# Optimization experiments

Measured on AMD Instinct MI355X. Metric: run time of the kernel, lower is better.

The kernel has to match this reference:

```python
import jax, jax.numpy as jnp
import numpy as np

H = 2048      # hidden
QL = 768      # q lora rank
KVL = 512     # kv lora rank
DR = 64       # rope dim
DN = 128      # nope head dim
NH = 16       # attention heads
NIH = 8       # indexer heads
IDX = 128     # indexer key dim
BS = 16       # batch
BLK = 128     # cache block size
BPS = 32      # blocks per sequence
NB = BS * BPS # total cache blocks
MAXKV = BPS * BLK  # 4096 kv slots per seq
TOPK = 1024   # sparse attention budget


def rmsnorm(v, g, eps=1e-6):
    return v * jax.lax.rsqrt(jnp.mean(v * v, -1, keepdims=True) + eps) * g


def layernorm(v, g, b, eps=1e-6):
    c = v - jnp.mean(v, -1, keepdims=True)
    return c * jax.lax.rsqrt(jnp.mean(c * c, -1, keepdims=True) + eps) * g + b


def rope(v, sin, cos):
    h = v.shape[-1] // 2
    rot = jnp.concatenate([-v[..., h:], v[..., :h]], -1)
    return v * cos + rot * sin


def setup_inputs() -> dict:
    key = jax.random.key(0)
    ks = jax.random.split(key, 16)
    s = 0.02  # weight init scale
    ang = jax.random.uniform(ks[5], (BS, 1, DR)) * 6.2831853
    return dict(
        x=jax.random.normal(ks[0], (BS, 1, H)),
        w_dq=jax.random.normal(ks[1], (H, QL)) * s,
        w_uq_qr=jax.random.normal(ks[2], (QL, NH * (DN + DR))) * s,
        w_uk=jax.random.normal(ks[3], (NH, DN, KVL)) * s,
        w_dkv_kr=jax.random.normal(ks[4], (H, KVL + DR)) * s,
        gamma_cq=jnp.ones((QL,)),
        gamma_ckv=jnp.ones((KVL,)),
        sin=jnp.sin(ang),
        cos=jnp.cos(ang),
        cache_index=jnp.arange(BS, dtype=jnp.int32) * MAXKV,
        kv_cache=jax.random.normal(ks[6], (NB, BLK, KVL)),
        kr_cache=jax.random.normal(ks[7], (NB, BLK, DR)),
        block_table=jnp.arange(BS * BPS, dtype=jnp.int32).reshape(BS, BPS),
        act_seqs=jnp.full((BS,), MAXKV, dtype=jnp.int32),
        w_idx_qb=jax.random.normal(ks[8], (QL, NIH * IDX)) * s,
        w_idx_k=jax.random.normal(ks[9], (H, IDX)) * s,
        w_idx_proj=jax.random.normal(ks[10], (QL, NIH)) * s,
        in_gamma_k=jnp.ones((IDX,)),
        in_beta_k=jnp.zeros((IDX,)),
        index_k_cache=jax.random.normal(ks[11], (NB, BLK, IDX)),
    )


def reference(x, w_dq, w_uq_qr, w_uk, w_dkv_kr, gamma_cq, gamma_ckv, sin, cos,
              cache_index, kv_cache, kr_cache, block_table, act_seqs,
              w_idx_qb, w_idx_k, w_idx_proj, in_gamma_k, in_beta_k, index_k_cache):
    bs = x.shape[0]
    xq = x[:, 0]                      # [bs, H] (decode, q_len=1)
    s0, c0 = sin[:, 0], cos[:, 0]     # [bs, DR]

    # --- low-rank Q path ---
    cq = rmsnorm(xq @ w_dq, gamma_cq)                           # [bs, QL]
    q = (cq @ w_uq_qr).reshape(bs, NH, DN + DR)
    q_nope, q_pe = q[..., :DN], q[..., DN:]
    q_pe = rope(q_pe, s0[:, None, :], c0[:, None, :])           # [bs, NH, DR]

    # --- latent KV path + cache write ---
    ckv_kr = xq @ w_dkv_kr
    ckv = rmsnorm(ckv_kr[:, :KVL], gamma_ckv)                   # [bs, KVL]
    kr = rope(ckv_kr[:, KVL:], s0, c0)                          # [bs, DR]
    kv_flat = kv_cache.reshape(NB * BLK, KVL).at[cache_index].set(ckv)
    kr_flat = kr_cache.reshape(NB * BLK, DR).at[cache_index].set(kr)

    # --- lightning indexer ---
    ki = layernorm(xq @ w_idx_k, in_gamma_k, in_beta_k)         # [bs, IDX]
    ik_flat = index_k_cache.reshape(NB * BLK, IDX).at[cache_index].set(ki)
    qi = (cq @ w_idx_qb).reshape(bs, NIH, IDX)
    head_w = cq @ w_idx_proj                                    # [bs, NIH]

    # paged gather: flat slot ids per sequence position
    pos = (block_table * BLK)[:, :, None] + jnp.arange(BLK, dtype=block_table.dtype)
    pos = pos.reshape(bs, MAXKV)                                # [bs, MAXKV]
    ki_all = ik_flat[pos]                                       # [bs, MAXKV, IDX]

    isc = jax.nn.relu(jnp.einsum('bhd,bnd->bhn', qi, ki_all))
    isc = jnp.einsum('bh,bhn->bn', head_w, isc) / jnp.sqrt(jnp.float32(IDX))
    mask = jnp.arange(MAXKV)[None, :] < act_seqs[:, None]
    isc = jnp.where(mask, isc, -1e9)
    top_s, top_i = jax.lax.top_k(isc, TOPK)                     # [bs, TOPK]

    sel = jnp.take_along_axis(pos, top_i, axis=1)               # [bs, TOPK]
    ckv_sel = kv_flat[sel]                                      # [bs, TOPK, KVL]
    kr_sel = kr_flat[sel]                                       # [bs, TOPK, DR]

    # --- absorbed MLA attention over selected tokens ---
    q_lat = jnp.einsum('bhd,hdc->bhc', q_nope, w_uk)            # [bs, NH, KVL]
    scale = 1.0 / np.sqrt(DN + DR)
    att = (jnp.einsum('bhc,bnc->bhn', q_lat, ckv_sel)
           + jnp.einsum('bhr,bnr->bhn', q_pe, kr_sel)) * scale
    att = jnp.where((top_s > -1e8)[:, None, :], att, -1e9)
    p = jax.nn.softmax(att, axis=-1)                            # [bs, NH, TOPK]
    o_lat = jnp.einsum('bhn,bnc->bhc', p, ckv_sel)              # [bs, NH, KVL]
    o = jnp.einsum('bhc,hdc->bhd', o_lat, w_uk)                 # [bs, NH, DN]
    return o.reshape(bs, 1, NH * DN)
```

## Files before the change

kernel.cpp:

```cpp
#include <hip/hip_runtime.h>

typedef unsigned int u32;

#define BS    16
#define HDIM  2048
#define QL    768
#define KVL   512
#define DR    64
#define DN    128
#define NH    16
#define NIH   8
#define IDXD  128
#define BLK   128
#define BPS   32
#define MAXKV 4096
#define TOPK  1024
#define NCH   32

__global__ void k_dproj(const float* __restrict__ x, const float* __restrict__ w_dq,
                        const float* __restrict__ w_dkv, const float* __restrict__ w_ik,
                        float* __restrict__ dpart){
  int tile = blockIdx.x, ks = blockIdx.y, t = threadIdx.x;
  __shared__ float xs[16*128];
  __shared__ float sred[8*32*17];
  int k0 = ks*128;
  for (int idx=t; idx<16*128; idx+=256){
    int bb=idx>>7, kk=idx&127;
    xs[idx] = x[bb*HDIM + k0 + kk];
  }
  const float* wp; int ld, c0, gbase;
  if (tile < 24){ wp=w_dq;  ld=768; c0=tile*32;      gbase=0; }
  else if (tile < 42){ wp=w_dkv; ld=576; c0=(tile-24)*32; gbase=768; }
  else { wp=w_ik;  ld=128; c0=(tile-42)*32; gbase=1344; }
  int cl = t&31, kg = t>>5;
  int col = c0 + cl;
  __syncthreads();
  float acc[16];
  #pragma unroll
  for (int bb=0;bb<16;bb++) acc[bb]=0.f;
  const float* wb = wp + (size_t)(k0 + kg*16)*ld + col;
  #pragma unroll 4
  for (int kk=0; kk<16; kk++){
    float wv = wb[(size_t)kk*ld];
    int kx = kg*16+kk;
    #pragma unroll
    for (int bb=0; bb<16; bb++) acc[bb] += xs[bb*128+kx]*wv;
  }
  #pragma unroll
  for (int bb=0;bb<16;bb++) sred[(kg*32+cl)*17+bb] = acc[bb];
  __syncthreads();
  for (int r=0; r<2; r++){
    int o = r*256 + t;
    int bb = o>>5, cl2 = o&31;
    float s=0.f;
    #pragma unroll
    for (int kg2=0; kg2<8; kg2++) s += sred[(kg2*32+cl2)*17+bb];
    dpart[((size_t)ks*16 + bb)*1472 + gbase + c0 + cl2] = s;
  }
}

__global__ void k_dfin(const float* __restrict__ dpart, const float* __restrict__ g_cq,
                       const float* __restrict__ g_ckv, const float* __restrict__ sinp,
                       const float* __restrict__ cosp, const float* __restrict__ g_ik,
                       const float* __restrict__ b_ik, const int* __restrict__ cidx,
                       float* __restrict__ cq, float* __restrict__ kvc,
                       float* __restrict__ krc, float* __restrict__ ikc){
  int b = blockIdx.x, sec = blockIdx.y, t = threadIdx.x;
  __shared__ float val[768];
  __shared__ float red[256];
  if (sec==0){
    for (int c=t; c<768; c+=256){
      float s = 0.f;
      for (int ks2=0; ks2<16; ks2++) s += dpart[((size_t)ks2*16+b)*1472 + c];
      val[c] = s;
    }
    __syncthreads();
    float c0v = val[t], c1v = val[t+256], c2v = val[t+512];
    red[t] = c0v*c0v + c1v*c1v + c2v*c2v;
    __syncthreads();
    for (int s=128;s>0;s>>=1){ if(t<s) red[t]+=red[t+s]; __syncthreads(); }
    float scq = 1.0f/sqrtf(red[0]/(float)QL + 1e-6f);
    cq[b*QL+t]     = c0v*scq*g_cq[t];
    cq[b*QL+t+256] = c1v*scq*g_cq[t+256];
    cq[b*QL+t+512] = c2v*scq*g_cq[t+512];
  } else if (sec==1){
    for (int c=t; c<576; c+=256){
      float s = 0.f;
      for (int ks2=0; ks2<16; ks2++) s += dpart[((size_t)ks2*16+b)*1472 + 768 + c];
      val[c] = s;
    }
    __syncthreads();
    float v0 = val[t], v1 = val[t+256];
    red[t] = v0*v0 + v1*v1;
    __syncthreads();
    for (int s=128;s>0;s>>=1){ if(t<s) red[t]+=red[t+s]; __syncthreads(); }
    float sckv = 1.0f/sqrtf(red[0]/(float)KVL + 1e-6f);
    int ci = cidx[b];
    kvc[(size_t)ci*KVL + t]     = v0*sckv*g_ckv[t];
    kvc[(size_t)ci*KVL + t+256] = v1*sckv*g_ckv[t+256];
    if (t<DR){
      float v = val[512+t];
      float rot = (t<32)? -val[512+t+32] : val[512+t-32];
      krc[(size_t)ci*DR + t] = v*cosp[b*DR+t] + rot*sinp[b*DR+t];
    }
  } else {
    for (int c=t; c<128; c+=256){
      float s = 0.f;
      for (int ks2=0; ks2<16; ks2++) s += dpart[((size_t)ks2*16+b)*1472 + 1344 + c];
      val[c] = s;
    }
    __syncthreads();
    red[t] = (t<128)? val[t] : 0.f;
    __syncthreads();
    for (int s=128;s>0;s>>=1){ if(t<s) red[t]+=red[t+s]; __syncthreads(); }
    float mean = red[0]/(float)IDXD;
    __syncthreads();
    float cc = (t<128)? (val[t]-mean) : 0.f;
    red[t] = cc*cc;
    __syncthreads();
    for (int s=128;s>0;s>>=1){ if(t<s) red[t]+=red[t+s]; __syncthreads(); }
    float var = red[0]/(float)IDXD;
    int ci = cidx[b];
    if (t<IDXD){
      ikc[(size_t)ci*IDXD + t] = cc/sqrtf(var+1e-6f)*g_ik[t] + b_ik[t];
    }
  }
}

__global__ void k_qall(const float* __restrict__ cq, const float* __restrict__ w_uq,
                       const float* __restrict__ w_qb, const float* __restrict__ w_pj,
                       float* __restrict__ qpart){
  int tile = blockIdx.x, ks = blockIdx.y, t = threadIdx.x;
  __shared__ float xs[16*192];
  __shared__ float sred[8*32*17];
  int k0 = ks*192;
  for (int idx=t; idx<16*192; idx+=256){
    int bb = idx/192, kk = idx - bb*192;
    xs[idx] = cq[bb*QL + k0 + kk];
  }
  const float* wp; int ld, c0, gbase, kind;
  if (tile < 96){ wp=w_uq; ld=3072; c0=tile*32; gbase=0; kind=0; }
  else if (tile < 128){ wp=w_qb; ld=1024; c0=(tile-96)*32; gbase=3072; kind=0; }
  else { wp=w_pj; ld=8; c0=0; gbase=4096; kind=1; }
  int cl = t&31, kg = t>>5;
  int col = c0 + cl;
  bool act = !(kind==1 && cl>=8);
  __syncthreads();
  float acc[16];
  #pragma unroll
  for (int bb=0;bb<16;bb++) acc[bb]=0.f;
  const float* wb = wp + (size_t)(k0 + kg*24)*ld + col;
  if (act){
    #pragma unroll 4
    for (int kk=0; kk<24; kk++){
      float wv = wb[(size_t)kk*ld];
      int kx = kg*24+kk;
      #pragma unroll
      for (int bb=0; bb<16; bb++) acc[bb] += xs[bb*192+kx]*wv;
    }
  }
  #pragma unroll
  for (int bb=0;bb<16;bb++) sred[(kg*32+cl)*17+bb] = acc[bb];
  __syncthreads();
  for (int r=0; r<2; r++){
    int o = r*256 + t;
    int bb = o>>5, cl2 = o&31;
    float s=0.f;
    #pragma unroll
    for (int kg2=0; kg2<8; kg2++) s += sred[(kg2*32+cl2)*17+bb];
    qpart[((size_t)ks*16 + bb)*4128 + gbase + c0 + cl2] = s;
  }
}

__global__ void k_qfin(const float* __restrict__ qpart, const float* __restrict__ sinp,
                       const float* __restrict__ cosp, float* __restrict__ qn,
                       float* __restrict__ qp, float* __restrict__ qi,
                       float* __restrict__ hw){
  int b=blockIdx.x, part=blockIdx.y, t=threadIdx.x;
  if (part<16){
    __shared__ float val[192];
    int h=part;
    if (t<192){
      int c = h*192 + t;
      float s=0.f;
      for (int ks=0; ks<4; ks++) s += qpart[((size_t)ks*16+b)*4128 + c];
      val[t]=s;
    }
    __syncthreads();
    if (t<192){
      int j=t;
      if (j<128) qn[(b*NH+h)*DN+j] = val[j];
      else {
        int d=j-128;
        float v=val[j];
        float rot = (d<32)? -val[160+d] : val[96+d];
        qp[(b*NH+h)*DR+d] = v*cosp[b*DR+d] + rot*sinp[b*DR+d];
      }
    }
  } else {
    for (int idx=t; idx<1032; idx+=256){
      int c = 3072+idx;
      float s=0.f;
      for (int ks=0; ks<4; ks++) s += qpart[((size_t)ks*16+b)*4128 + c];
      if (idx<1024) qi[b*1024 + idx] = s;
      else hw[b*NIH + idx-1024] = s;
    }
  }
}

__global__ void k_qlat(const float* __restrict__ qn, const float* __restrict__ wuk,
                       float* __restrict__ ql){
  int h=blockIdx.x, ct=blockIdx.y, t=threadIdx.x;
  __shared__ float qs[16*128];
  __shared__ float sred[4*64*17];
  for (int idx=t; idx<2048; idx+=256)
    qs[idx] = qn[((idx>>7)*NH+h)*DN + (idx&127)];
  int cl=t&63, kg=t>>6;
  int col=ct*64+cl;
  __syncthreads();
  float acc[16];
  #pragma unroll
  for (int bb=0;bb<16;bb++) acc[bb]=0.f;
  const float* wb = wuk + ((size_t)h*DN + kg*32)*KVL + col;
  #pragma unroll 4
  for (int kk=0;kk<32;kk++){
    float wv = wb[(size_t)kk*KVL];
    int kx = kg*32+kk;
    #pragma unroll
    for (int bb=0;bb<16;bb++) acc[bb]+=qs[bb*128+kx]*wv;
  }
  #pragma unroll
  for (int bb=0;bb<16;bb++) sred[(kg*64+cl)*17+bb]=acc[bb];
  __syncthreads();
  for (int r=0;r<4;r++){
    int o=r*256+t;
    int bb=o>>6, cl2=o&63;
    float s=0.f;
    #pragma unroll
    for (int kg2=0;kg2<4;kg2++) s+=sred[(kg2*64+cl2)*17+bb];
    ql[((size_t)bb*NH+h)*KVL + ct*64+cl2] = s;
  }
}

__global__ void k_isc(const float* __restrict__ qi, const float* __restrict__ hw,
                      const float* __restrict__ ikc, const int* __restrict__ btab,
                      const int* __restrict__ aseq, float* __restrict__ isc){
  int b=blockIdx.x, jb=blockIdx.y, t=threadIdx.x;
  __shared__ float K[64*129];
  __shared__ float qs[NIH*130];
  __shared__ float hs[NIH];
  __shared__ float red[64*4];
  int blk = btab[b*BPS+jb];
  for (int idx=t; idx<NIH*IDXD; idx+=256){ int h2=idx>>7, d=idx&127; qs[h2*130+d]=qi[b*1024+idx]; }
  if (t<NIH) hs[t]=hw[b*NIH+t];
  const float4* k4 = (const float4*)(ikc + (size_t)blk*BLK*IDXD);
  int as = aseq[b];
  int r = t>>2, hp = t&3;
  for (int half=0; half<2; half++){
    __syncthreads();
    for (int it=0; it<8; it++){
      int idx = it*256 + t;
      int rr = idx>>5, c4 = idx&31;
      float4 v = k4[(half*64+rr)*32 + c4];
      float* dst = &K[rr*129 + c4*4];
      dst[0]=v.x; dst[1]=v.y; dst[2]=v.z; dst[3]=v.w;
    }
    __syncthreads();
    float s0=0.f, s1=0.f;
    const float* Kr = &K[r*129];
    const float* q0 = &qs[hp*130];
    const float* q1 = &qs[(hp+4)*130];
    for (int d=0; d<IDXD; d++){
      float kv = Kr[d];
      s0 += q0[d]*kv; s1 += q1[d]*kv;
    }
    red[r*4+hp] = hs[hp]*fmaxf(s0,0.f) + hs[hp+4]*fmaxf(s1,0.f);
    __syncthreads();
    if (t<64){
      float sc = (red[t*4]+red[t*4+1]+red[t*4+2]+red[t*4+3]) * 0.08838834764831845f;
      int n = jb*BLK + half*64 + t;
      if (n >= as) sc = -1e9f;
      isc[b*MAXKV + n] = sc;
    }
  }
}

__global__ void k_topk(const float* __restrict__ isc, const int* __restrict__ btab,
                       int* __restrict__ selp, float* __restrict__ sels){
  int b=blockIdx.x, t=threadIdx.x;
  int lane = t&63, wv = t>>6;
  __shared__ u32 su[MAXKV];
  __shared__ u32 hist[256];
  __shared__ u32 cum[256];
  __shared__ u32 wtot[4];
  __shared__ u32 sh_b;
  for (int k2=0;k2<16;k2++){
    int i=k2*256+t;
    u32 bits=__float_as_uint(isc[b*MAXKV+i]);
    su[i] = (bits & 0x80000000u) ? ~bits : (bits | 0x80000000u);
  }
  u32 prefix=0u, need=1024u;
  for (int shift=24; shift>=0; shift-=8){
    hist[t]=0u;
    __syncthreads();
    u32 hm = (shift==24)? 0u : (0xFFFFFFFFu << (shift+8));
    for (int j=0;j<16;j++){
      u32 u = su[t*16+j];
      if ((u & hm) == prefix) atomicAdd(&hist[(u>>shift)&255u], 1u);
    }
    __syncthreads();
    u32 v = hist[wv*64+lane];
    for (int off=1; off<64; off<<=1){
      u32 tmp = __shfl_down(v, off);
      if (lane + off < 64) v += tmp;
    }
    if (lane==0) wtot[wv]=v;
    __syncthreads();
    u32 add=0u;
    for (int w2=wv+1; w2<4; w2++) add += wtot[w2];
    v += add;
    cum[wv*64+lane] = v;
    __syncthreads();
    int bin = wv*64+lane;
    u32 nxt = (bin<255)? cum[bin+1] : 0u;
    if (v>=need && nxt<need) sh_b = (u32)bin;
    __syncthreads();
    u32 B = sh_b;
    u32 aboveB = (B<255u)? cum[B+1] : 0u;
    need -= aboveB;
    prefix |= (B<<shift);
    __syncthreads();
  }
  u32 T = prefix;
  u32 cG=0u,cE=0u;
  for (int j=0;j<16;j++){ u32 u=su[t*16+j]; cG += (u>T)?1u:0u; cE += (u==T)?1u:0u; }
  u32 packed = (cG<<16) | cE;
  u32 v = packed;
  for (int off=1; off<64; off<<=1){
    u32 tmp = __shfl_up(v, off);
    if (lane >= off) v += tmp;
  }
  if (lane==63) wtot[wv]=v;
  __syncthreads();
  u32 add=0u;
  for (int w2=0; w2<wv; w2++) add += wtot[w2];
  u32 excl = v + add - packed;
  u32 total = wtot[0]+wtot[1]+wtot[2]+wtot[3];
  u32 mGT = total>>16;
  u32 keepEq = 1024u - mGT;
  u32 gG = excl>>16, gE = excl&0xFFFFu;
  for (int j=0;j<16;j++){
    int i=t*16+j; u32 u=su[i];
    int slot=-1;
    if (u>T) slot=(int)(gG++);
    else if (u==T){ u32 r2=gE++; if (r2<keepEq) slot=(int)(mGT+r2); }
    if (slot>=0){
      int pos = btab[b*BPS + (i>>7)]*BLK + (i&127);
      selp[b*TOPK+slot]=pos;
      sels[b*TOPK+slot]=isc[b*MAXKV+i];
    }
  }
}

__global__ __launch_bounds__(256, 2)
void k_fgat(const float* __restrict__ qlat, const float* __restrict__ qpe,
            const float* __restrict__ kvc, const float* __restrict__ krc,
            const int* __restrict__ selp, const float* __restrict__ sels,
            float* __restrict__ opart, float* __restrict__ mch,
            float* __restrict__ lch){
  int ch=blockIdx.x, b=blockIdx.y, t=threadIdx.x;
  __shared__ float K[32*580];
  int lane31 = t&31;
  int sp_l   = selp[b*TOPK + ch*32 + lane31];
  float sv_l = sels[b*TOPK + ch*32 + lane31];
  const float4* kv4 = (const float4*)kvc;
  const float4* kr4 = (const float4*)krc;
  float4 rA[18];
  #pragma unroll
  for (int j=0;j<18;j++){
    int idx=j*256+t, r=idx/144, c=idx-r*144;
    int row = __shfl(sp_l, r, 64);
    rA[j] = (c<128)? kv4[(size_t)row*128 + c] : kr4[(size_t)row*16 + (c-128)];
  }
  int h = t>>4, kc = t&15;
  const float4* ql4 = (const float4*)(qlat + ((size_t)b*NH+h)*KVL);
  const float4* qp4 = (const float4*)(qpe  + ((size_t)b*NH+h)*DR);
  float4 qreg[9];
  #pragma unroll
  for (int j=0;j<9;j++){
    int g = kc*9 + j;
    qreg[j] = (g<128)? ql4[g] : qp4[g-128];
  }
  #pragma unroll
  for (int j=0;j<18;j++){
    int idx=j*256+t, r=idx/144, c=idx-r*144;
    ((float4*)&K[r*580])[c] = rA[j];
  }
  __syncthreads();
  const float scale = 0.07216878364870323f;
  float pa=0.f, pb=0.f;
  for (int r=0;r<32;r++){
    const float4* Kc = (const float4*)&K[r*580 + kc*36];
    float s=0.f;
    #pragma unroll
    for (int j=0;j<9;j++){
      float4 kv=Kc[j], q=qreg[j];
      s += kv.x*q.x + kv.y*q.y + kv.z*q.z + kv.w*q.w;
    }
    #pragma unroll
    for (int mm=1;mm<16;mm<<=1) s += __shfl_xor(s, mm, 16);
    float svr = __shfl(sv_l, r, 64);
    float val = (svr > -1e8f)? s*scale : -1e9f;
    if (r<16) pa = (kc==r)?      val : pa;
    else      pb = (kc==(r-16))? val : pb;
  }
  float m2 = fmaxf(pa, pb);
  #pragma unroll
  for (int mm=1;mm<16;mm<<=1) m2 = fmaxf(m2, __shfl_xor(m2, mm, 16));
  pa = expf(pa - m2); pb = expf(pb - m2);
  float l2 = pa + pb;
  #pragma unroll
  for (int mm=1;mm<16;mm<<=1) l2 += __shfl_xor(l2, mm, 16);
  int l6 = t&63;
  float4 a0[4], a1[4];
  #pragma unroll
  for (int hq=0;hq<4;hq++){
    a0[hq].x=a0[hq].y=a0[hq].z=a0[hq].w=0.f;
    a1[hq].x=a1[hq].y=a1[hq].z=a1[hq].w=0.f;
  }
  for (int r=0;r<32;r++){
    const float4* Vr = (const float4*)&K[r*580];
    float4 v0 = Vr[l6], v1 = Vr[64+l6];
    float ps = (r<16)? pa : pb;
    int srcl = (r&15);
    float p0 = __shfl(ps, srcl,      64);
    float p1 = __shfl(ps, 16+srcl,   64);
    float p2 = __shfl(ps, 32+srcl,   64);
    float p3 = __shfl(ps, 48+srcl,   64);
    a0[0].x+=p0*v0.x; a0[0].y+=p0*v0.y; a0[0].z+=p0*v0.z; a0[0].w+=p0*v0.w;
    a1[0].x+=p0*v1.x; a1[0].y+=p0*v1.y; a1[0].z+=p0*v1.z; a1[0].w+=p0*v1.w;
    a0[1].x+=p1*v0.x; a0[1].y+=p1*v0.y; a0[1].z+=p1*v0.z; a0[1].w+=p1*v0.w;
    a1[1].x+=p1*v1.x; a1[1].y+=p1*v1.y; a1[1].z+=p1*v1.z; a1[1].w+=p1*v1.w;
    a0[2].x+=p2*v0.x; a0[2].y+=p2*v0.y; a0[2].z+=p2*v0.z; a0[2].w+=p2*v0.w;
    a1[2].x+=p2*v1.x; a1[2].y+=p2*v1.y; a1[2].z+=p2*v1.z; a1[2].w+=p2*v1.w;
    a0[3].x+=p3*v0.x; a0[3].y+=p3*v0.y; a0[3].z+=p3*v0.z; a0[3].w+=p3*v0.w;
    a1[3].x+=p3*v1.x; a1[3].y+=p3*v1.y; a1[3].z+=p3*v1.z; a1[3].w+=p3*v1.w;
  }
  int wv = t>>6;
  #pragma unroll
  for (int hq=0;hq<4;hq++){
    int hh = wv*4 + hq;
    float4* dst = (float4*)(opart + (((size_t)(b*NCH+ch))*NH + hh)*KVL);
    dst[l6]    = a0[hq];
    dst[64+l6] = a1[hq];
  }
  if (kc==0){
    mch[(b*NCH+ch)*16 + h] = m2;
    lch[(b*NCH+ch)*16 + h] = l2;
  }
}

__global__ void k_comb(const float* __restrict__ opart, const float* __restrict__ mch,
                       const float* __restrict__ lch, const float* __restrict__ wuk,
                       float* __restrict__ out){
  int b=blockIdx.x, h=blockIdx.y, t=threadIdx.x;
  __shared__ float sOl[KVL];
  __shared__ float sCoef[NCH];
  __shared__ float sInvL;
  if (t<NCH){
    float mv = mch[(b*NCH+t)*16+h];
    float lv = lch[(b*NCH+t)*16+h];
    float M = mv;
    for (int off=1; off<NCH; off<<=1) M = fmaxf(M, __shfl_xor(M, off, NCH));
    float coef = expf(mv - M);
    float Lp = lv*coef;
    for (int off=1; off<NCH; off<<=1) Lp += __shfl_xor(Lp, off, NCH);
    sCoef[t] = coef;
    if (t==0) sInvL = 1.0f/Lp;
  }
  __syncthreads();
  for (int c=t; c<KVL; c+=128){
    float s=0.f;
    for (int ch=0; ch<NCH; ch++)
      s += opart[(((size_t)(b*NCH+ch))*NH + h)*KVL + c] * sCoef[ch];
    sOl[c] = s*sInvL;
  }
  __syncthreads();
  const float4* w4 = (const float4*)(wuk + ((size_t)(h*DN)+t)*KVL);
  const float4* o4 = (const float4*)sOl;
  float a=0.f;
  for (int v=0; v<128; v++){
    float4 w = w4[v]; float4 o = o4[v];
    a += w.x*o.x + w.y*o.y + w.z*o.z + w.w*o.w;
  }
  out[b*(NH*DN) + h*DN + t] = a;
}

extern "C" void kernel_launch(void* const* d_in, const int* in_sizes, int n_in,
                              void* d_out, int out_size, void* d_ws, size_t ws_size,
                              hipStream_t stream){
  const float* x        =(const float*)d_in[0];
  const float* w_dq     =(const float*)d_in[1];
  const float* w_uq_qr  =(const float*)d_in[2];
  const float* w_uk     =(const float*)d_in[3];
  const float* w_dkv_kr =(const float*)d_in[4];
  const float* g_cq     =(const float*)d_in[5];
  const float* g_ckv    =(const float*)d_in[6];
  const float* sinp     =(const float*)d_in[7];
  const float* cosp     =(const float*)d_in[8];
  const int*   cidx     =(const int*)d_in[9];
  float*       kvc      =(float*)d_in[10];
  float*       krc      =(float*)d_in[11];
  const int*   btab     =(const int*)d_in[12];
  const int*   aseq     =(const int*)d_in[13];
  const float* w_idx_qb =(const float*)d_in[14];
  const float* w_idx_k  =(const float*)d_in[15];
  const float* w_idx_pj =(const float*)d_in[16];
  const float* g_ik     =(const float*)d_in[17];
  const float* b_ik     =(const float*)d_in[18];
  float*       ikc      =(float*)d_in[19];

  float* ws    = (float*)d_ws;
  float* cq    = ws;
  float* qnope = ws + 12288;
  float* qpe   = ws + 45056;
  float* qlat  = ws + 61440;
  float* qi    = ws + 192512;
  float* hw    = ws + 208896;
  float* isc   = ws + 209024;
  int*   selp  = (int*)(ws + 274560);
  float* sels  = ws + 290944;
  float* dpart = ws + 307328;
  float* qpart = ws + 684160;
  float* mch   = ws + 948352;
  float* lch   = ws + 956544;
  float* opart = ws + 964736;

  k_dproj<<<dim3(46,16),  dim3(256),0,stream>>>(x,w_dq,w_dkv_kr,w_idx_k,dpart);
  k_dfin <<<dim3(BS,3),   dim3(256),0,stream>>>(dpart,g_cq,g_ckv,sinp,cosp,g_ik,b_ik,cidx,cq,kvc,krc,ikc);
  k_qall <<<dim3(129,4),  dim3(256),0,stream>>>(cq,w_uq_qr,w_idx_qb,w_idx_pj,qpart);
  k_qfin <<<dim3(BS,17),  dim3(256),0,stream>>>(qpart,sinp,cosp,qnope,qpe,qi,hw);
  k_qlat <<<dim3(16,8),   dim3(256),0,stream>>>(qnope,w_uk,qlat);
  k_isc  <<<dim3(BS,BPS), dim3(256),0,stream>>>(qi,hw,ikc,btab,aseq,isc);
  k_topk <<<dim3(BS),     dim3(256),0,stream>>>(isc,btab,selp,sels);
  k_fgat <<<dim3(NCH,BS), dim3(256),0,stream>>>(qlat,qpe,kvc,krc,selp,sels,opart,mch,lch);
  k_comb <<<dim3(BS,NH),  dim3(128),0,stream>>>(opart,mch,lch,w_uk,(float*)d_out);
}
```

Measured before the change: 344.7 us.

## Fuse q-latent projection into qfin, stop writing cache, tweak isc/topk

Folds the per-head w_uk projection into k_qfin, removing the k_qlat launch and the q_nope round trip. The new kv/kr/index-key rows are now written to workspace and substituted on read in k_isc and k_fgat, instead of being scattered into the input caches. k_isc also gains float4 shared-memory loads with padded rows, and k_topk uses 16 privatized histogram copies with strided element ownership to cut atomic contention. The fused qlat computation redoes the w_uk read once per batch row (16x more weight traffic) in exchange for one fewer launch.

```diff
diff --git a/kernel.cpp b/kernel.cpp
--- a/kernel.cpp
+++ b/kernel.cpp
@@ -62,9 +62,9 @@
 __global__ void k_dfin(const float* __restrict__ dpart, const float* __restrict__ g_cq,
                        const float* __restrict__ g_ckv, const float* __restrict__ sinp,
                        const float* __restrict__ cosp, const float* __restrict__ g_ik,
-                       const float* __restrict__ b_ik, const int* __restrict__ cidx,
-                       float* __restrict__ cq, float* __restrict__ kvc,
-                       float* __restrict__ krc, float* __restrict__ ikc){
+                       const float* __restrict__ b_ik,
+                       float* __restrict__ cq, float* __restrict__ newkv,
+                       float* __restrict__ newkr, float* __restrict__ newik){
   int b = blockIdx.x, sec = blockIdx.y, t = threadIdx.x;
   __shared__ float val[768];
   __shared__ float red[256];
@@ -95,13 +95,12 @@
     __syncthreads();
     for (int s=128;s>0;s>>=1){ if(t<s) red[t]+=red[t+s]; __syncthreads(); }
     float sckv = 1.0f/sqrtf(red[0]/(float)KVL + 1e-6f);
-    int ci = cidx[b];
-    kvc[(size_t)ci*KVL + t]     = v0*sckv*g_ckv[t];
-    kvc[(size_t)ci*KVL + t+256] = v1*sckv*g_ckv[t+256];
+    newkv[(size_t)b*KVL + t]     = v0*sckv*g_ckv[t];
+    newkv[(size_t)b*KVL + t+256] = v1*sckv*g_ckv[t+256];
     if (t<DR){
       float v = val[512+t];
       float rot = (t<32)? -val[512+t+32] : val[512+t-32];
-      krc[(size_t)ci*DR + t] = v*cosp[b*DR+t] + rot*sinp[b*DR+t];
+      newkr[(size_t)b*DR + t] = v*cosp[b*DR+t] + rot*sinp[b*DR+t];
     }
   } else {
     for (int c=t; c<128; c+=256){
@@ -120,9 +119,8 @@
     __syncthreads();
     for (int s=128;s>0;s>>=1){ if(t<s) red[t]+=red[t+s]; __syncthreads(); }
     float var = red[0]/(float)IDXD;
-    int ci = cidx[b];
     if (t<IDXD){
-      ikc[(size_t)ci*IDXD + t] = cc/sqrtf(var+1e-6f)*g_ik[t] + b_ik[t];
+      newik[(size_t)b*IDXD + t] = cc/sqrtf(var+1e-6f)*g_ik[t] + b_ik[t];
     }
   }
 }
@@ -173,9 +171,9 @@
 }
 
 __global__ void k_qfin(const float* __restrict__ qpart, const float* __restrict__ sinp,
-                       const float* __restrict__ cosp, float* __restrict__ qn,
-                       float* __restrict__ qp, float* __restrict__ qi,
-                       float* __restrict__ hw){
+                       const float* __restrict__ cosp, const float* __restrict__ wuk,
+                       float* __restrict__ qp, float* __restrict__ qlat,
+                       float* __restrict__ qi, float* __restrict__ hw){
   int b=blockIdx.x, part=blockIdx.y, t=threadIdx.x;
   if (part<16){
     __shared__ float val[192];
@@ -187,16 +185,22 @@
       val[t]=s;
     }
     __syncthreads();
-    if (t<192){
-      int j=t;
-      if (j<128) qn[(b*NH+h)*DN+j] = val[j];
-      else {
-        int d=j-128;
-        float v=val[j];
-        float rot = (d<32)? -val[160+d] : val[96+d];
-        qp[(b*NH+h)*DR+d] = v*cosp[b*DR+d] + rot*sinp[b*DR+d];
-      }
-    }
+    if (t>=128 && t<192){
+      int d=t-128;
+      float v=val[t];
+      float rot = (d<32)? -val[160+d] : val[96+d];
+      qp[(b*NH+h)*DR+d] = v*cosp[b*DR+d] + rot*sinp[b*DR+d];
+    }
+    float a0=0.f, a1=0.f;
+    const float* w = wuk + (size_t)h*DN*KVL;
+    #pragma unroll 4
+    for (int d=0; d<128; d++){
+      float qv = val[d];
+      a0 += qv * w[(size_t)d*KVL + t];
+      a1 += qv * w[(size_t)d*KVL + t + 256];
+    }
+    qlat[((size_t)b*NH+h)*KVL + t]       = a0;
+    qlat[((size_t)b*NH+h)*KVL + t + 256] = a1;
   } else {
     for (int idx=t; idx<1032; idx+=256){
       int c = 3072+idx;
@@ -208,52 +212,21 @@
   }
 }
 
-__global__ void k_qlat(const float* __restrict__ qn, const float* __restrict__ wuk,
-                       float* __restrict__ ql){
-  int h=blockIdx.x, ct=blockIdx.y, t=threadIdx.x;
-  __shared__ float qs[16*128];
-  __shared__ float sred[4*64*17];
-  for (int idx=t; idx<2048; idx+=256)
-    qs[idx] = qn[((idx>>7)*NH+h)*DN + (idx&127)];
-  int cl=t&63, kg=t>>6;
-  int col=ct*64+cl;
-  __syncthreads();
-  float acc[16];
-  #pragma unroll
-  for (int bb=0;bb<16;bb++) acc[bb]=0.f;
-  const float* wb = wuk + ((size_t)h*DN + kg*32)*KVL + col;
-  #pragma unroll 4
-  for (int kk=0;kk<32;kk++){
-    float wv = wb[(size_t)kk*KVL];
-    int kx = kg*32+kk;
-    #pragma unroll
-    for (int bb=0;bb<16;bb++) acc[bb]+=qs[bb*128+kx]*wv;
-  }
-  #pragma unroll
-  for (int bb=0;bb<16;bb++) sred[(kg*64+cl)*17+bb]=acc[bb];
-  __syncthreads();
-  for (int r=0;r<4;r++){
-    int o=r*256+t;
-    int bb=o>>6, cl2=o&63;
-    float s=0.f;
-    #pragma unroll
-    for (int kg2=0;kg2<4;kg2++) s+=sred[(kg2*64+cl2)*17+bb];
-    ql[((size_t)bb*NH+h)*KVL + ct*64+cl2] = s;
-  }
-}
-
 __global__ void k_isc(const float* __restrict__ qi, const float* __restrict__ hw,
                       const float* __restrict__ ikc, const int* __restrict__ btab,
-                      const int* __restrict__ aseq, float* __restrict__ isc){
+                      const int* __restrict__ aseq, const int* __restrict__ cidx,
+                      const float* __restrict__ newik, float* __restrict__ isc){
   int b=blockIdx.x, jb=blockIdx.y, t=threadIdx.x;
-  __shared__ float K[64*129];
-  __shared__ float qs[NIH*130];
+  __shared__ float K[64*132];
+  __shared__ float qs[NIH*132];
   __shared__ float hs[NIH];
   __shared__ float red[64*4];
   int blk = btab[b*BPS+jb];
-  for (int idx=t; idx<NIH*IDXD; idx+=256){ int h2=idx>>7, d=idx&127; qs[h2*130+d]=qi[b*1024+idx]; }
+  int ci  = cidx[b];
+  for (int idx=t; idx<NIH*IDXD; idx+=256){ int h2=idx>>7, d=idx&127; qs[h2*132+d]=qi[b*1024+idx]; }
   if (t<NIH) hs[t]=hw[b*NIH+t];
-  const float4* k4 = (const float4*)(ikc + (size_t)blk*BLK*IDXD);
+  const float4* k4   = (const float4*)(ikc + (size_t)blk*BLK*IDXD);
+  const float4* nik4 = (const float4*)(newik + (size_t)b*IDXD);
   int as = aseq[b];
   int r = t>>2, hp = t&3;
   for (int half=0; half<2; half++){
@@ -261,18 +234,21 @@
     for (int it=0; it<8; it++){
       int idx = it*256 + t;
       int rr = idx>>5, c4 = idx&31;
-      float4 v = k4[(half*64+rr)*32 + c4];
-      float* dst = &K[rr*129 + c4*4];
-      dst[0]=v.x; dst[1]=v.y; dst[2]=v.z; dst[3]=v.w;
+      int grow = blk*BLK + half*64 + rr;
+      float4 v = (grow==ci)? nik4[c4] : k4[(half*64+rr)*32 + c4];
+      ((float4*)&K[rr*132])[c4] = v;
     }
     __syncthreads();
     float s0=0.f, s1=0.f;
-    const float* Kr = &K[r*129];
-    const float* q0 = &qs[hp*130];
-    const float* q1 = &qs[(hp+4)*130];
-    for (int d=0; d<IDXD; d++){
-      float kv = Kr[d];
-      s0 += q0[d]*kv; s1 += q1[d]*kv;
+    const float4* Kr = (const float4*)&K[r*132];
+    const float4* q0 = (const float4*)&qs[hp*132];
+    const float4* q1 = (const float4*)&qs[(hp+4)*132];
+    for (int d=0; d<32; d++){
+      float4 kv=Kr[d], a=q0[d], c=q1[d];
+      s0 += a.x*kv.x; s1 += c.x*kv.x;
+      s0 += a.y*kv.y; s1 += c.y*kv.y;
+      s0 += a.z*kv.z; s1 += c.z*kv.z;
+      s0 += a.w*kv.w; s1 += c.w*kv.w;
     }
     red[r*4+hp] = hs[hp]*fmaxf(s0,0.f) + hs[hp+4]*fmaxf(s1,0.f);
     __syncthreads();
@@ -290,26 +266,30 @@
   int b=blockIdx.x, t=threadIdx.x;
   int lane = t&63, wv = t>>6;
   __shared__ u32 su[MAXKV];
-  __shared__ u32 hist[256];
+  __shared__ u32 hist[16*256];
   __shared__ u32 cum[256];
   __shared__ u32 wtot[4];
   __shared__ u32 sh_b;
-  for (int k2=0;k2<16;k2++){
-    int i=k2*256+t;
+  int hc = (t&15)*256;
+  for (int j=0;j<16;j++){
+    int i=j*256+t;
     u32 bits=__float_as_uint(isc[b*MAXKV+i]);
     su[i] = (bits & 0x80000000u) ? ~bits : (bits | 0x80000000u);
   }
   u32 prefix=0u, need=1024u;
   for (int shift=24; shift>=0; shift-=8){
-    hist[t]=0u;
+    for (int j=t;j<16*256;j+=256) hist[j]=0u;
     __syncthreads();
     u32 hm = (shift==24)? 0u : (0xFFFFFFFFu << (shift+8));
     for (int j=0;j<16;j++){
-      u32 u = su[t*16+j];
-      if ((u & hm) == prefix) atomicAdd(&hist[(u>>shift)&255u], 1u);
-    }
-    __syncthreads();
-    u32 v = hist[wv*64+lane];
+      u32 u = su[j*256+t];
+      if ((u & hm) == prefix) atomicAdd(&hist[hc + ((u>>shift)&255u)], 1u);
+    }
+    __syncthreads();
+    int bin = wv*64+lane;
+    u32 v = 0u;
+    #pragma unroll
+    for (int cpy=0;cpy<16;cpy++) v += hist[cpy*256+bin];
     for (int off=1; off<64; off<<=1){
       u32 tmp = __shfl_down(v, off);
       if (lane + off < 64) v += tmp;
@@ -319,9 +299,8 @@
     u32 add=0u;
     for (int w2=wv+1; w2<4; w2++) add += wtot[w2];
     v += add;
-    cum[wv*64+lane] = v;
-    __syncthreads();
-    int bin = wv*64+lane;
+    cum[bin] = v;
+    __syncthreads();
     u32 nxt = (bin<255)? cum[bin+1] : 0u;
     if (v>=need && nxt<need) sh_b = (u32)bin;
     __syncthreads();
@@ -333,7 +312,7 @@
   }
   u32 T = prefix;
   u32 cG=0u,cE=0u;
-  for (int j=0;j<16;j++){ u32 u=su[t*16+j]; cG += (u>T)?1u:0u; cE += (u==T)?1u:0u; }
+  for (int j=0;j<16;j++){ u32 u=su[j*256+t]; cG += (u>T)?1u:0u; cE += (u==T)?1u:0u; }
   u32 packed = (cG<<16) | cE;
   u32 v = packed;
   for (int off=1; off<64; off<<=1){
@@ -350,7 +329,7 @@
   u32 keepEq = 1024u - mGT;
   u32 gG = excl>>16, gE = excl&0xFFFFu;
   for (int j=0;j<16;j++){
-    int i=t*16+j; u32 u=su[i];
+    int i=j*256+t; u32 u=su[i];
     int slot=-1;
     if (u>T) slot=(int)(gG++);
     else if (u==T){ u32 r2=gE++; if (r2<keepEq) slot=(int)(mGT+r2); }
@@ -366,6 +345,8 @@
 void k_fgat(const float* __restrict__ qlat, const float* __restrict__ qpe,
             const float* __restrict__ kvc, const float* __restrict__ krc,
             const int* __restrict__ selp, const float* __restrict__ sels,
+            const int* __restrict__ cidx, const float* __restrict__ newkv,
+            const float* __restrict__ newkr,
             float* __restrict__ opart, float* __restrict__ mch,
             float* __restrict__ lch){
   int ch=blockIdx.x, b=blockIdx.y, t=threadIdx.x;
@@ -373,14 +354,20 @@
   int lane31 = t&31;
   int sp_l   = selp[b*TOPK + ch*32 + lane31];
   float sv_l = sels[b*TOPK + ch*32 + lane31];
-  const float4* kv4 = (const float4*)kvc;
-  const float4* kr4 = (const float4*)krc;
+  int ci = cidx[b];
+  const float4* kv4  = (const float4*)kvc;
+  const float4* kr4  = (const float4*)krc;
+  const float4* nkv4 = (const float4*)newkv;
+  const float4* nkr4 = (const float4*)newkr;
   float4 rA[18];
   #pragma unroll
   for (int j=0;j<18;j++){
     int idx=j*256+t, r=idx/144, c=idx-r*144;
     int row = __shfl(sp_l, r, 64);
-    rA[j] = (c<128)? kv4[(size_t)row*128 + c] : kr4[(size_t)row*16 + (c-128)];
+    const float4* src;
+    if (c<128) src = (row==ci)? (nkv4 + (size_t)b*128 + c) : (kv4 + (size_t)row*128 + c);
+    else       src = (row==ci)? (nkr4 + (size_t)b*16 + (c-128)) : (kr4 + (size_t)row*16 + (c-128));
+    rA[j] = *src;
   }
   int h = t>>4, kc = t&15;
   const float4* ql4 = (const float4*)(qlat + ((size_t)b*NH+h)*KVL);
@@ -509,8 +496,8 @@
   const float* sinp     =(const float*)d_in[7];
   const float* cosp     =(const float*)d_in[8];
   const int*   cidx     =(const int*)d_in[9];
-  float*       kvc      =(float*)d_in[10];
-  float*       krc      =(float*)d_in[11];
+  const float* kvc      =(const float*)d_in[10];
+  const float* krc      =(const float*)d_in[11];
   const int*   btab     =(const int*)d_in[12];
   const int*   aseq     =(const int*)d_in[13];
   const float* w_idx_qb =(const float*)d_in[14];
@@ -518,31 +505,32 @@
   const float* w_idx_pj =(const float*)d_in[16];
   const float* g_ik     =(const float*)d_in[17];
   const float* b_ik     =(const float*)d_in[18];
-  float*       ikc      =(float*)d_in[19];
+  const float* ikc      =(const float*)d_in[19];
 
   float* ws    = (float*)d_ws;
   float* cq    = ws;
-  float* qnope = ws + 12288;
-  float* qpe   = ws + 45056;
-  float* qlat  = ws + 61440;
-  float* qi    = ws + 192512;
-  float* hw    = ws + 208896;
-  float* isc   = ws + 209024;
-  int*   selp  = (int*)(ws + 274560);
-  float* sels  = ws + 290944;
-  float* dpart = ws + 307328;
-  float* qpart = ws + 684160;
-  float* mch   = ws + 948352;
-  float* lch   = ws + 956544;
-  float* opart = ws + 964736;
+  float* qpe   = ws + 12288;
+  float* qlat  = ws + 28672;
+  float* qi    = ws + 159744;
+  float* hw    = ws + 176128;
+  float* isc   = ws + 176256;
+  int*   selp  = (int*)(ws + 241792);
+  float* sels  = ws + 258176;
+  float* dpart = ws + 274560;
+  float* qpart = ws + 651392;
+  float* mch   = ws + 915584;
+  float* lch   = ws + 923776;
+  float* opart = ws + 931968;
+  float* newkv = ws + 5126272;
+  float* newkr = ws + 5134464;
+  float* newik = ws + 5135488;
 
   k_dproj<<<dim3(46,16),  dim3(256),0,stream>>>(x,w_dq,w_dkv_kr,w_idx_k,dpart);
-  k_dfin <<<dim3(BS,3),   dim3(256),0,stream>>>(dpart,g_cq,g_ckv,sinp,cosp,g_ik,b_ik,cidx,cq,kvc,krc,ikc);
+  k_dfin <<<dim3(BS,3),   dim3(256),0,stream>>>(dpart,g_cq,g_ckv,sinp,cosp,g_ik,b_ik,cq,newkv,newkr,newik);
   k_qall <<<dim3(129,4),  dim3(256),0,stream>>>(cq,w_uq_qr,w_idx_qb,w_idx_pj,qpart);
-  k_qfin <<<dim3(BS,17),  dim3(256),0,stream>>>(qpart,sinp,cosp,qnope,qpe,qi,hw);
-  k_qlat <<<dim3(16,8),   dim3(256),0,stream>>>(qnope,w_uk,qlat);
-  k_isc  <<<dim3(BS,BPS), dim3(256),0,stream>>>(qi,hw,ikc,btab,aseq,isc);
+  k_qfin <<<dim3(BS,17),  dim3(256),0,stream>>>(qpart,sinp,cosp,w_uk,qpe,qlat,qi,hw);
+  k_isc  <<<dim3(BS,BPS), dim3(256),0,stream>>>(qi,hw,ikc,btab,aseq,cidx,newik,isc);
   k_topk <<<dim3(BS),     dim3(256),0,stream>>>(isc,btab,selp,sels);
-  k_fgat <<<dim3(NCH,BS), dim3(256),0,stream>>>(qlat,qpe,kvc,krc,selp,sels,opart,mch,lch);
+  k_fgat <<<dim3(NCH,BS), dim3(256),0,stream>>>(qlat,qpe,kvc,krc,selp,sels,cidx,newkv,newkr,opart,mch,lch);
   k_comb <<<dim3(BS,NH),  dim3(128),0,stream>>>(opart,mch,lch,w_uk,(float*)d_out);
 }
```

New measurement: 352.9 us. 2.4% more time.

## Stop mutating caches, widen top-k block, vectorize index scoring, restructure gather attention

Applied to the files above, without the earlier changes.

The new KV, rope-key and indexer-key rows now go to workspace buffers and are substituted on read wherever the row index equals cache_index, so the input caches are no longer written in place. The top-k kernel moves from 256 to 1024 threads with 16 privatized histogram copies to reduce atomic contention. Index scoring switches to float4 shared-memory reads with padded rows. The gather-attention kernel computes two heads per thread and hands the softmax probabilities through shared memory instead of shuffles. These are several unrelated changes, and the per-row cache_index comparisons add a little work to both gathers.

```diff
diff --git a/kernel.cpp b/kernel.cpp
--- a/kernel.cpp
+++ b/kernel.cpp
@@ -62,9 +62,9 @@
 __global__ void k_dfin(const float* __restrict__ dpart, const float* __restrict__ g_cq,
                        const float* __restrict__ g_ckv, const float* __restrict__ sinp,
                        const float* __restrict__ cosp, const float* __restrict__ g_ik,
-                       const float* __restrict__ b_ik, const int* __restrict__ cidx,
-                       float* __restrict__ cq, float* __restrict__ kvc,
-                       float* __restrict__ krc, float* __restrict__ ikc){
+                       const float* __restrict__ b_ik,
+                       float* __restrict__ cq, float* __restrict__ newkv,
+                       float* __restrict__ newkr, float* __restrict__ newik){
   int b = blockIdx.x, sec = blockIdx.y, t = threadIdx.x;
   __shared__ float val[768];
   __shared__ float red[256];
@@ -95,13 +95,12 @@
     __syncthreads();
     for (int s=128;s>0;s>>=1){ if(t<s) red[t]+=red[t+s]; __syncthreads(); }
     float sckv = 1.0f/sqrtf(red[0]/(float)KVL + 1e-6f);
-    int ci = cidx[b];
-    kvc[(size_t)ci*KVL + t]     = v0*sckv*g_ckv[t];
-    kvc[(size_t)ci*KVL + t+256] = v1*sckv*g_ckv[t+256];
+    newkv[(size_t)b*KVL + t]     = v0*sckv*g_ckv[t];
+    newkv[(size_t)b*KVL + t+256] = v1*sckv*g_ckv[t+256];
     if (t<DR){
       float v = val[512+t];
       float rot = (t<32)? -val[512+t+32] : val[512+t-32];
-      krc[(size_t)ci*DR + t] = v*cosp[b*DR+t] + rot*sinp[b*DR+t];
+      newkr[(size_t)b*DR + t] = v*cosp[b*DR+t] + rot*sinp[b*DR+t];
     }
   } else {
     for (int c=t; c<128; c+=256){
@@ -120,9 +119,8 @@
     __syncthreads();
     for (int s=128;s>0;s>>=1){ if(t<s) red[t]+=red[t+s]; __syncthreads(); }
     float var = red[0]/(float)IDXD;
-    int ci = cidx[b];
     if (t<IDXD){
-      ikc[(size_t)ci*IDXD + t] = cc/sqrtf(var+1e-6f)*g_ik[t] + b_ik[t];
+      newik[(size_t)b*IDXD + t] = cc/sqrtf(var+1e-6f)*g_ik[t] + b_ik[t];
     }
   }
 }
@@ -244,16 +242,19 @@
 
 __global__ void k_isc(const float* __restrict__ qi, const float* __restrict__ hw,
                       const float* __restrict__ ikc, const int* __restrict__ btab,
-                      const int* __restrict__ aseq, float* __restrict__ isc){
+                      const int* __restrict__ aseq, const int* __restrict__ cidx,
+                      const float* __restrict__ newik, float* __restrict__ isc){
   int b=blockIdx.x, jb=blockIdx.y, t=threadIdx.x;
-  __shared__ float K[64*129];
-  __shared__ float qs[NIH*130];
+  __shared__ float K[64*132];
+  __shared__ float qs[NIH*132];
   __shared__ float hs[NIH];
   __shared__ float red[64*4];
   int blk = btab[b*BPS+jb];
-  for (int idx=t; idx<NIH*IDXD; idx+=256){ int h2=idx>>7, d=idx&127; qs[h2*130+d]=qi[b*1024+idx]; }
+  int ci  = cidx[b];
+  for (int idx=t; idx<NIH*IDXD; idx+=256){ int h2=idx>>7, d=idx&127; qs[h2*132+d]=qi[b*1024+idx]; }
   if (t<NIH) hs[t]=hw[b*NIH+t];
-  const float4* k4 = (const float4*)(ikc + (size_t)blk*BLK*IDXD);
+  const float4* k4   = (const float4*)(ikc + (size_t)blk*BLK*IDXD);
+  const float4* nik4 = (const float4*)(newik + (size_t)b*IDXD);
   int as = aseq[b];
   int r = t>>2, hp = t&3;
   for (int half=0; half<2; half++){
@@ -261,18 +262,21 @@
     for (int it=0; it<8; it++){
       int idx = it*256 + t;
       int rr = idx>>5, c4 = idx&31;
-      float4 v = k4[(half*64+rr)*32 + c4];
-      float* dst = &K[rr*129 + c4*4];
-      dst[0]=v.x; dst[1]=v.y; dst[2]=v.z; dst[3]=v.w;
+      int grow = blk*BLK + half*64 + rr;
+      float4 v = (grow==ci)? nik4[c4] : k4[(half*64+rr)*32 + c4];
+      ((float4*)&K[rr*132])[c4] = v;
     }
     __syncthreads();
     float s0=0.f, s1=0.f;
-    const float* Kr = &K[r*129];
-    const float* q0 = &qs[hp*130];
-    const float* q1 = &qs[(hp+4)*130];
-    for (int d=0; d<IDXD; d++){
-      float kv = Kr[d];
-      s0 += q0[d]*kv; s1 += q1[d]*kv;
+    const float4* Kr = (const float4*)&K[r*132];
+    const float4* q0 = (const float4*)&qs[hp*132];
+    const float4* q1 = (const float4*)&qs[(hp+4)*132];
+    for (int d=0; d<32; d++){
+      float4 kv=Kr[d], a=q0[d], c=q1[d];
+      s0 += a.x*kv.x; s1 += c.x*kv.x;
+      s0 += a.y*kv.y; s1 += c.y*kv.y;
+      s0 += a.z*kv.z; s1 += c.z*kv.z;
+      s0 += a.w*kv.w; s1 += c.w*kv.w;
     }
     red[r*4+hp] = hs[hp]*fmaxf(s0,0.f) + hs[hp+4]*fmaxf(s1,0.f);
     __syncthreads();
@@ -285,45 +289,54 @@
   }
 }
 
-__global__ void k_topk(const float* __restrict__ isc, const int* __restrict__ btab,
-                       int* __restrict__ selp, float* __restrict__ sels){
+__global__ __launch_bounds__(1024)
+void k_topk(const float* __restrict__ isc, const int* __restrict__ btab,
+            int* __restrict__ selp, float* __restrict__ sels){
   int b=blockIdx.x, t=threadIdx.x;
   int lane = t&63, wv = t>>6;
   __shared__ u32 su[MAXKV];
-  __shared__ u32 hist[256];
+  __shared__ u32 hist[16*256];
   __shared__ u32 cum[256];
-  __shared__ u32 wtot[4];
+  __shared__ u32 wtot[16];
   __shared__ u32 sh_b;
-  for (int k2=0;k2<16;k2++){
-    int i=k2*256+t;
+  int hc = (t&15)*256;
+  for (int j=0;j<4;j++){
+    int i=j*1024+t;
     u32 bits=__float_as_uint(isc[b*MAXKV+i]);
     su[i] = (bits & 0x80000000u) ? ~bits : (bits | 0x80000000u);
   }
   u32 prefix=0u, need=1024u;
   for (int shift=24; shift>=0; shift-=8){
-    hist[t]=0u;
+    for (int j=t;j<16*256;j+=1024) hist[j]=0u;
     __syncthreads();
     u32 hm = (shift==24)? 0u : (0xFFFFFFFFu << (shift+8));
-    for (int j=0;j<16;j++){
-      u32 u = su[t*16+j];
-      if ((u & hm) == prefix) atomicAdd(&hist[(u>>shift)&255u], 1u);
-    }
-    __syncthreads();
-    u32 v = hist[wv*64+lane];
-    for (int off=1; off<64; off<<=1){
-      u32 tmp = __shfl_down(v, off);
-      if (lane + off < 64) v += tmp;
-    }
-    if (lane==0) wtot[wv]=v;
-    __syncthreads();
-    u32 add=0u;
-    for (int w2=wv+1; w2<4; w2++) add += wtot[w2];
-    v += add;
-    cum[wv*64+lane] = v;
-    __syncthreads();
-    int bin = wv*64+lane;
-    u32 nxt = (bin<255)? cum[bin+1] : 0u;
-    if (v>=need && nxt<need) sh_b = (u32)bin;
+    for (int j=0;j<4;j++){
+      u32 u = su[j*1024+t];
+      if ((u & hm) == prefix) atomicAdd(&hist[hc + ((u>>shift)&255u)], 1u);
+    }
+    __syncthreads();
+    u32 v=0u;
+    if (t<256){
+      #pragma unroll
+      for (int cpy=0;cpy<16;cpy++) v += hist[cpy*256+t];
+      for (int off=1; off<64; off<<=1){
+        u32 tmp = __shfl_down(v, off);
+        if (lane + off < 64) v += tmp;
+      }
+      if (lane==0) wtot[wv]=v;
+    }
+    __syncthreads();
+    if (t<256){
+      u32 add=0u;
+      for (int w2=wv+1; w2<4; w2++) add += wtot[w2];
+      v += add;
+      cum[t]=v;
+    }
+    __syncthreads();
+    if (t<256){
+      u32 nxt = (t<255)? cum[t+1] : 0u;
+      if (v>=need && nxt<need) sh_b = (u32)t;
+    }
     __syncthreads();
     u32 B = sh_b;
     u32 aboveB = (B<255u)? cum[B+1] : 0u;
@@ -333,7 +346,7 @@
   }
   u32 T = prefix;
   u32 cG=0u,cE=0u;
-  for (int j=0;j<16;j++){ u32 u=su[t*16+j]; cG += (u>T)?1u:0u; cE += (u==T)?1u:0u; }
+  for (int j=0;j<4;j++){ u32 u=su[j*1024+t]; cG += (u>T)?1u:0u; cE += (u==T)?1u:0u; }
   u32 packed = (cG<<16) | cE;
   u32 v = packed;
   for (int off=1; off<64; off<<=1){
@@ -345,12 +358,14 @@
   u32 add=0u;
   for (int w2=0; w2<wv; w2++) add += wtot[w2];
   u32 excl = v + add - packed;
-  u32 total = wtot[0]+wtot[1]+wtot[2]+wtot[3];
+  u32 total = 0u;
+  #pragma unroll
+  for (int w2=0; w2<16; w2++) total += wtot[w2];
   u32 mGT = total>>16;
   u32 keepEq = 1024u - mGT;
   u32 gG = excl>>16, gE = excl&0xFFFFu;
-  for (int j=0;j<16;j++){
-    int i=t*16+j; u32 u=su[i];
+  for (int j=0;j<4;j++){
+    int i=j*1024+t; u32 u=su[i];
     int slot=-1;
     if (u>T) slot=(int)(gG++);
     else if (u==T){ u32 r2=gE++; if (r2<keepEq) slot=(int)(mGT+r2); }
@@ -366,30 +381,42 @@
 void k_fgat(const float* __restrict__ qlat, const float* __restrict__ qpe,
             const float* __restrict__ kvc, const float* __restrict__ krc,
             const int* __restrict__ selp, const float* __restrict__ sels,
+            const int* __restrict__ cidx, const float* __restrict__ newkv,
+            const float* __restrict__ newkr,
             float* __restrict__ opart, float* __restrict__ mch,
             float* __restrict__ lch){
   int ch=blockIdx.x, b=blockIdx.y, t=threadIdx.x;
   __shared__ float K[32*580];
+  __shared__ float sP[32*16];
   int lane31 = t&31;
   int sp_l   = selp[b*TOPK + ch*32 + lane31];
   float sv_l = sels[b*TOPK + ch*32 + lane31];
-  const float4* kv4 = (const float4*)kvc;
-  const float4* kr4 = (const float4*)krc;
+  int ci = cidx[b];
+  const float4* kv4  = (const float4*)kvc;
+  const float4* kr4  = (const float4*)krc;
+  const float4* nkv4 = (const float4*)newkv;
+  const float4* nkr4 = (const float4*)newkr;
   float4 rA[18];
   #pragma unroll
   for (int j=0;j<18;j++){
     int idx=j*256+t, r=idx/144, c=idx-r*144;
     int row = __shfl(sp_l, r, 64);
-    rA[j] = (c<128)? kv4[(size_t)row*128 + c] : kr4[(size_t)row*16 + (c-128)];
-  }
-  int h = t>>4, kc = t&15;
-  const float4* ql4 = (const float4*)(qlat + ((size_t)b*NH+h)*KVL);
-  const float4* qp4 = (const float4*)(qpe  + ((size_t)b*NH+h)*DR);
-  float4 qreg[9];
+    const float4* src;
+    if (c<128) src = (row==ci)? (nkv4 + (size_t)b*128 + c) : (kv4 + (size_t)row*128 + c);
+    else       src = (row==ci)? (nkr4 + (size_t)b*16 + (c-128)) : (kr4 + (size_t)row*16 + (c-128));
+    rA[j] = *src;
+  }
+  int hp = t>>5, sub = (t>>4)&1, kc = t&15;
+  const float4* qlA = (const float4*)(qlat + ((size_t)b*NH+hp)*KVL);
+  const float4* qpA = (const float4*)(qpe  + ((size_t)b*NH+hp)*DR);
+  const float4* qlB = (const float4*)(qlat + ((size_t)b*NH+hp+8)*KVL);
+  const float4* qpB = (const float4*)(qpe  + ((size_t)b*NH+hp+8)*DR);
+  float4 qa[9], qb[9];
   #pragma unroll
   for (int j=0;j<9;j++){
     int g = kc*9 + j;
-    qreg[j] = (g<128)? ql4[g] : qp4[g-128];
+    qa[j] = (g<128)? qlA[g] : qpA[g-128];
+    qb[j] = (g<128)? qlB[g] : qpB[g-128];
   }
   #pragma unroll
   for (int j=0;j<18;j++){
@@ -399,29 +426,51 @@
   __syncthreads();
   const float scale = 0.07216878364870323f;
   float pa=0.f, pb=0.f;
-  for (int r=0;r<32;r++){
+  for (int rl=0; rl<16; rl++){
+    int r = sub*16 + rl;
     const float4* Kc = (const float4*)&K[r*580 + kc*36];
-    float s=0.f;
+    float sA=0.f, sB=0.f;
     #pragma unroll
     for (int j=0;j<9;j++){
-      float4 kv=Kc[j], q=qreg[j];
-      s += kv.x*q.x + kv.y*q.y + kv.z*q.z + kv.w*q.w;
-    }
-    #pragma unroll
-    for (int mm=1;mm<16;mm<<=1) s += __shfl_xor(s, mm, 16);
+      float4 kv=Kc[j];
+      sA += kv.x*qa[j].x + kv.y*qa[j].y + kv.z*qa[j].z + kv.w*qa[j].w;
+      sB += kv.x*qb[j].x + kv.y*qb[j].y + kv.z*qb[j].z + kv.w*qb[j].w;
+    }
+    #pragma unroll
+    for (int mm=1;mm<16;mm<<=1){
+      sA += __shfl_xor(sA, mm, 16);
+      sB += __shfl_xor(sB, mm, 16);
+    }
     float svr = __shfl(sv_l, r, 64);
-    float val = (svr > -1e8f)? s*scale : -1e9f;
-    if (r<16) pa = (kc==r)?      val : pa;
-    else      pb = (kc==(r-16))? val : pb;
-  }
-  float m2 = fmaxf(pa, pb);
-  #pragma unroll
-  for (int mm=1;mm<16;mm<<=1) m2 = fmaxf(m2, __shfl_xor(m2, mm, 16));
-  pa = expf(pa - m2); pb = expf(pb - m2);
-  float l2 = pa + pb;
-  #pragma unroll
-  for (int mm=1;mm<16;mm<<=1) l2 += __shfl_xor(l2, mm, 16);
-  int l6 = t&63;
+    float vA = (svr > -1e8f)? sA*scale : -1e9f;
+    float vB = (svr > -1e8f)? sB*scale : -1e9f;
+    if (kc==rl){ pa = vA; pb = vB; }
+  }
+  float mA = pa, mB = pb;
+  #pragma unroll
+  for (int mm=1;mm<32;mm<<=1){
+    mA = fmaxf(mA, __shfl_xor(mA, mm, 32));
+    mB = fmaxf(mB, __shfl_xor(mB, mm, 32));
+  }
+  pa = expf(pa - mA); pb = expf(pb - mB);
+  float lA = pa, lB = pb;
+  #pragma unroll
+  for (int mm=1;mm<32;mm<<=1){
+    lA += __shfl_xor(lA, mm, 32);
+    lB += __shfl_xor(lB, mm, 32);
+  }
+  int r31 = sub*16 + kc;
+  sP[r31*16 + hp]     = pa;
+  sP[r31*16 + hp + 8] = pb;
+  if (r31==0){
+    mch[(b*NCH+ch)*16 + hp]     = mA;
+    mch[(b*NCH+ch)*16 + hp + 8] = mB;
+    lch[(b*NCH+ch)*16 + hp]     = lA;
+    lch[(b*NCH+ch)*16 + hp + 8] = lB;
+  }
+  __syncthreads();
+  int l6 = t&63, hg = t>>6;
+  const float4* sP4 = (const float4*)sP;
   float4 a0[4], a1[4];
   #pragma unroll
   for (int hq=0;hq<4;hq++){
@@ -431,32 +480,22 @@
   for (int r=0;r<32;r++){
     const float4* Vr = (const float4*)&K[r*580];
     float4 v0 = Vr[l6], v1 = Vr[64+l6];
-    float ps = (r<16)? pa : pb;
-    int srcl = (r&15);
-    float p0 = __shfl(ps, srcl,      64);
-    float p1 = __shfl(ps, 16+srcl,   64);
-    float p2 = __shfl(ps, 32+srcl,   64);
-    float p3 = __shfl(ps, 48+srcl,   64);
-    a0[0].x+=p0*v0.x; a0[0].y+=p0*v0.y; a0[0].z+=p0*v0.z; a0[0].w+=p0*v0.w;
-    a1[0].x+=p0*v1.x; a1[0].y+=p0*v1.y; a1[0].z+=p0*v1.z; a1[0].w+=p0*v1.w;
-    a0[1].x+=p1*v0.x; a0[1].y+=p1*v0.y; a0[1].z+=p1*v0.z; a0[1].w+=p1*v0.w;
-    a1[1].x+=p1*v1.x; a1[1].y+=p1*v1.y; a1[1].z+=p1*v1.z; a1[1].w+=p1*v1.w;
-    a0[2].x+=p2*v0.x; a0[2].y+=p2*v0.y; a0[2].z+=p2*v0.z; a0[2].w+=p2*v0.w;
-    a1[2].x+=p2*v1.x; a1[2].y+=p2*v1.y; a1[2].z+=p2*v1.z; a1[2].w+=p2*v1.w;
-    a0[3].x+=p3*v0.x; a0[3].y+=p3*v0.y; a0[3].z+=p3*v0.z; a0[3].w+=p3*v0.w;
-    a1[3].x+=p3*v1.x; a1[3].y+=p3*v1.y; a1[3].z+=p3*v1.z; a1[3].w+=p3*v1.w;
-  }
-  int wv = t>>6;
+    float4 p4 = sP4[r*4 + hg];
+    a0[0].x+=p4.x*v0.x; a0[0].y+=p4.x*v0.y; a0[0].z+=p4.x*v0.z; a0[0].w+=p4.x*v0.w;
+    a1[0].x+=p4.x*v1.x; a1[0].y+=p4.x*v1.y; a1[0].z+=p4.x*v1.z; a1[0].w+=p4.x*v1.w;
+    a0[1].x+=p4.y*v0.x; a0[1].y+=p4.y*v0.y; a0[1].z+=p4.y*v0.z; a0[1].w+=p4.y*v0.w;
+    a1[1].x+=p4.y*v1.x; a1[1].y+=p4.y*v1.y; a1[1].z+=p4.y*v1.z; a1[1].w+=p4.y*v1.w;
+    a0[2].x+=p4.z*v0.x; a0[2].y+=p4.z*v0.y; a0[2].z+=p4.z*v0.z; a0[2].w+=p4.z*v0.w;
+    a1[2].x+=p4.z*v1.x; a1[2].y+=p4.z*v1.y; a1[2].z+=p4.z*v1.z; a1[2].w+=p4.z*v1.w;
+    a0[3].x+=p4.w*v0.x; a0[3].y+=p4.w*v0.y; a0[3].z+=p4.w*v0.z; a0[3].w+=p4.w*v0.w;
+    a1[3].x+=p4.w*v1.x; a1[3].y+=p4.w*v1.y; a1[3].z+=p4.w*v1.z; a1[3].w+=p4.w*v1.w;
+  }
   #pragma unroll
   for (int hq=0;hq<4;hq++){
-    int hh = wv*4 + hq;
+    int hh = hg*4 + hq;
     float4* dst = (float4*)(opart + (((size_t)(b*NCH+ch))*NH + hh)*KVL);
     dst[l6]    = a0[hq];
     dst[64+l6] = a1[hq];
-  }
-  if (kc==0){
-    mch[(b*NCH+ch)*16 + h] = m2;
-    lch[(b*NCH+ch)*16 + h] = l2;
   }
 }
 
@@ -509,8 +548,8 @@
   const float* sinp     =(const float*)d_in[7];
   const float* cosp     =(const float*)d_in[8];
   const int*   cidx     =(const int*)d_in[9];
-  float*       kvc      =(float*)d_in[10];
-  float*       krc      =(float*)d_in[11];
+  const float* kvc      =(const float*)d_in[10];
+  const float* krc      =(const float*)d_in[11];
   const int*   btab     =(const int*)d_in[12];
   const int*   aseq     =(const int*)d_in[13];
   const float* w_idx_qb =(const float*)d_in[14];
@@ -518,7 +557,7 @@
   const float* w_idx_pj =(const float*)d_in[16];
   const float* g_ik     =(const float*)d_in[17];
   const float* b_ik     =(const float*)d_in[18];
-  float*       ikc      =(float*)d_in[19];
+  const float* ikc      =(const float*)d_in[19];
 
   float* ws    = (float*)d_ws;
   float* cq    = ws;
@@ -535,14 +574,17 @@
   float* mch   = ws + 948352;
   float* lch   = ws + 956544;
   float* opart = ws + 964736;
+  float* newkv = ws + 5159040;
+  float* newkr = ws + 5167232;
+  float* newik = ws + 5168256;
 
   k_dproj<<<dim3(46,16),  dim3(256),0,stream>>>(x,w_dq,w_dkv_kr,w_idx_k,dpart);
-  k_dfin <<<dim3(BS,3),   dim3(256),0,stream>>>(dpart,g_cq,g_ckv,sinp,cosp,g_ik,b_ik,cidx,cq,kvc,krc,ikc);
+  k_dfin <<<dim3(BS,3),   dim3(256),0,stream>>>(dpart,g_cq,g_ckv,sinp,cosp,g_ik,b_ik,cq,newkv,newkr,newik);
   k_qall <<<dim3(129,4),  dim3(256),0,stream>>>(cq,w_uq_qr,w_idx_qb,w_idx_pj,qpart);
   k_qfin <<<dim3(BS,17),  dim3(256),0,stream>>>(qpart,sinp,cosp,qnope,qpe,qi,hw);
   k_qlat <<<dim3(16,8),   dim3(256),0,stream>>>(qnope,w_uk,qlat);
-  k_isc  <<<dim3(BS,BPS), dim3(256),0,stream>>>(qi,hw,ikc,btab,aseq,isc);
-  k_topk <<<dim3(BS),     dim3(256),0,stream>>>(isc,btab,selp,sels);
-  k_fgat <<<dim3(NCH,BS), dim3(256),0,stream>>>(qlat,qpe,kvc,krc,selp,sels,opart,mch,lch);
+  k_isc  <<<dim3(BS,BPS), dim3(256),0,stream>>>(qi,hw,ikc,btab,aseq,cidx,newik,isc);
+  k_topk <<<dim3(BS),     dim3(1024),0,stream>>>(isc,btab,selp,sels);
+  k_fgat <<<dim3(NCH,BS), dim3(256),0,stream>>>(qlat,qpe,kvc,krc,selp,sels,cidx,newkv,newkr,opart,mch,lch);
   k_comb <<<dim3(BS,NH),  dim3(128),0,stream>>>(opart,mch,lch,w_uk,(float*)d_out);
 }
```

After: 331.7 us. 1.04x faster.
